# Optimization experiments

Measured on AMD Instinct MI355X. Metric: run time of the kernel, lower is better.

## Reference

```python
import jax, jax.numpy as jnp
import numpy as np

T, D, K, V, NB = 32768, 256, 16, 16, 2
H = K * V  # hidden size; must equal D for the residual x + y

def phi(x):
    return 1.0 + jax.nn.elu(x)

def _layernorm(x, w, b, eps=1e-5):
    m = x.mean(-1, keepdims=True)
    v = ((x - m) ** 2).mean(-1, keepdims=True)
    return (x - m) * jax.lax.rsqrt(v + eps) * w + b

def _combine(a, b):
    # reset-wrapped associative update: right element's start flag zeroes the left carry
    pa, sa, za = a
    pb, sb, zb = b
    keep = jnp.logical_not(pb)
    return (jnp.logical_or(pa, pb), keep * sa + sb, keep * za + zb)

def _block(x, start, s0, z0, Wk, Wq, Wv, bv, Wskip, bskip, Wm1, bm1, Wm2, bm2, Wm3, bm3, lnw, lnb):
    k = phi(x @ Wk.T)                                   # [T,K]
    q = phi(x @ Wq.T)                                   # [T,K]
    v = x @ Wv.T + bv                                   # [T,V]
    kv = jnp.einsum('ti,tj->tij', k, v)                 # [T,K,V]
    s = jnp.concatenate([s0, kv], axis=0)               # [T+1,K,V]
    z = jnp.concatenate([z0, k[:, None, :]], axis=0)    # [T+1,1,K]
    st = jnp.concatenate([jnp.zeros((1, 1, 1), bool), start.reshape(-1, 1, 1)], axis=0)
    _, s, z = jax.lax.associative_scan(_combine, (st, s, z), axis=0)
    s, z = s[1:], z[1:]
    numer = jnp.einsum('tij,ti->tj', s, q)              # [T,V]
    denom = jnp.einsum('tzi,tj->tz', z, q).clip(1e-6)   # [T,1] (faithful to source einsum)
    out = numer / denom                                 # [T,V]
    h = jax.nn.leaky_relu(out @ Wm1.T + bm1)
    h = jax.nn.leaky_relu(h @ Wm2.T + bm2)
    h = h @ Wm3.T + bm3
    return _layernorm(h + (x @ Wskip.T + bskip), lnw, lnb)

def _forward(x, start, s0, z0, Wk, Wq, Wv, bv, Wskip, bskip, Wm1, bm1, Wm2, bm2, Wm3, bm3, lnw, lnb):
    y = x
    for i in range(NB):  # small fixed layer loop
        y = _block(x, start, s0[i], z0[i], Wk[i], Wq[i], Wv[i], bv[i], Wskip[i], bskip[i],
                   Wm1[i], bm1[i], Wm2[i], bm2[i], Wm3[i], bm3[i], lnw[i], lnb[i])
        x = x + y
    return y

def setup_inputs() -> dict:
    key = jax.random.key(0)
    ks = jax.random.split(key, 12)
    g = lambda k, shp, fan: jax.random.normal(k, shp, jnp.float32) * (fan ** -0.5)
    return dict(
        x=jax.random.normal(ks[0], (T, D), jnp.float32),
        start=jax.random.randint(ks[1], (T,), 0, 2).astype(bool),
        s0=jnp.zeros((NB, 1, K, V), jnp.float32),
        z0=jnp.zeros((NB, 1, 1, K), jnp.float32),
        Wk=g(ks[2], (NB, K, D), D), Wq=g(ks[3], (NB, K, D), D),
        Wv=g(ks[4], (NB, V, D), D), bv=jnp.zeros((NB, V), jnp.float32),
        Wskip=g(ks[5], (NB, H, D), D), bskip=jnp.zeros((NB, H), jnp.float32),
        Wm1=g(ks[6], (NB, H, V), V), bm1=jnp.zeros((NB, H), jnp.float32),
        Wm2=g(ks[7], (NB, H, H), H), bm2=jnp.zeros((NB, H), jnp.float32),
        Wm3=g(ks[8], (NB, H, H), H), bm3=jnp.zeros((NB, H), jnp.float32),
        ln_w=jnp.ones((NB, H), jnp.float32), ln_b=jnp.zeros((NB, H), jnp.float32),
    )

def reference(x, start, s0, z0, Wk, Wq, Wv, bv, Wskip, bskip, Wm1, bm1, Wm2, bm2, Wm3, bm3, ln_w, ln_b):
    return _forward(x, start, s0, z0, Wk, Wq, Wv, bv, Wskip, bskip, Wm1, bm1, Wm2, bm2, Wm3, bm3, ln_w, ln_b)
```

## Files before the change

kernel.cpp:

```cpp
#include <hip/hip_runtime.h>
#include <hip/hip_bf16.h>
#include <cstdint>

#define TT   32768
#define DD   256
#define KV   16
#define NBLK 2
#define HH   256
#define CH   64
#define NCH  (TT / CH)

typedef __attribute__((ext_vector_type(8))) short bf16x8;
typedef __attribute__((ext_vector_type(4))) float f32x4;

__device__ __forceinline__ float phi_f(float x)  { return x > 0.f ? x + 1.f : expf(x); }
__device__ __forceinline__ float lrelu_f(float x){ return x > 0.f ? x : 0.01f * x; }
__device__ __forceinline__ unsigned short f2bf(float f) {
  unsigned u = __float_as_uint(f);
  u += 0x7fffu + ((u >> 16) & 1u);
  return (unsigned short)(u >> 16);
}
__device__ __forceinline__ float bf2f(unsigned short h) {
  return __uint_as_float(((unsigned)h) << 16);
}

__global__ void k_detect(const void* __restrict__ startp, int* __restrict__ flags) {
  int stride = gridDim.x * blockDim.x;
  for (int t = blockIdx.x * blockDim.x + threadIdx.x; t < TT / 4; t += stride) {
    unsigned u = ((const unsigned*)startp)[t];
    if (u > 1u) atomicOr(&flags[0], 1);
    float f = ((const float*)startp)[t];
    if (!(f == 0.f || f == 1.f)) atomicOr(&flags[1], 1);
  }
}

__global__ void k_canon(const void* __restrict__ startp, const int* __restrict__ flags,
                        float* __restrict__ start_f) {
  int v32 = flags[0], vf = flags[1];
  int stride = gridDim.x * blockDim.x;
  for (int t = blockIdx.x * blockDim.x + threadIdx.x; t < TT; t += stride) {
    bool s;
    if (v32 == 0)     s = ((const unsigned*)startp)[t] != 0u;
    else if (vf == 0) s = ((const float*)startp)[t] != 0.f;
    else              s = ((const unsigned char*)startp)[t] != 0;
    start_f[t] = s ? 1.f : 0.f;
  }
}

__global__ __launch_bounds__(256) void k_cvtbig(
    const float* __restrict__ s0, const float* __restrict__ s1, const float* __restrict__ s2,
    unsigned short* __restrict__ d0, unsigned short* __restrict__ d1,
    unsigned short* __restrict__ d2, int n) {
  int i = (blockIdx.x * 256 + threadIdx.x) * 8;
  const float* s; unsigned short* d;
  if (i < n)            { s = s0; d = d0; }
  else if (i < 2 * n)   { s = s1; d = d1; i -= n; }
  else if (i < 3 * n)   { s = s2; d = d2; i -= 2 * n; }
  else return;
  float4 a = *(const float4*)(s + i);
  float4 b = *(const float4*)(s + i + 4);
  float vals[8] = {a.x, a.y, a.z, a.w, b.x, b.y, b.z, b.w};
  bf16x8 t;
#pragma unroll
  for (int j = 0; j < 8; j++) t[j] = (short)f2bf(vals[j]);
  *(bf16x8*)(d + i) = t;
}

__global__ __launch_bounds__(256) void k_cvtproj(
    const float* __restrict__ Wk, const float* __restrict__ Wq, const float* __restrict__ Wv,
    unsigned short* __restrict__ wh, unsigned short* __restrict__ wl) {
  int t8 = blockIdx.x * 256 + threadIdx.x;
  if (t8 >= NBLK * 48 * 256 / 8) return;
  int e = t8 * 8;
  int b = e / (48 * 256);
  int rem = e - b * 48 * 256;
  int o = rem / (16 * 256);
  int nr = rem - o * 16 * 256;
  const float* src = (o == 0 ? Wk : o == 1 ? Wq : Wv) + b * 16 * 256 + nr;
  float4 a = *(const float4*)src;
  float4 c = *(const float4*)(src + 4);
  float vals[8] = {a.x, a.y, a.z, a.w, c.x, c.y, c.z, c.w};
  bf16x8 th, tl;
#pragma unroll
  for (int j = 0; j < 8; j++) {
    unsigned short h = f2bf(vals[j]);
    th[j] = (short)h;
    tl[j] = (short)f2bf(vals[j] - bf2f(h));
  }
  *(bf16x8*)(wh + e) = th;
  *(bf16x8*)(wl + e) = tl;
}

__global__ __launch_bounds__(256) void k_proj2(
    const float* __restrict__ x,
    const unsigned short* __restrict__ wh, const unsigned short* __restrict__ wl,
    const float* __restrict__ bv,
    float* __restrict__ kout, float* __restrict__ qout, float* __restrict__ vout) {
  __shared__ unsigned short xh[64 * 256];
  __shared__ unsigned short xl[64 * 256];
  int tid = threadIdx.x, wg = blockIdx.x;
  size_t rbase = (size_t)wg * 64;
  const float* xs = x + rbase * DD;
#pragma unroll
  for (int i = 0; i < 8; i++) {
    int idx = tid + i * 256;
    int row = idx >> 5, c8 = idx & 31;
    const float* p = xs + row * DD + c8 * 8;
    float4 a = *(const float4*)p;
    float4 b = *(const float4*)(p + 4);
    float vals[8] = {a.x, a.y, a.z, a.w, b.x, b.y, b.z, b.w};
    bf16x8 th, tl;
#pragma unroll
    for (int j = 0; j < 8; j++) {
      unsigned short h = f2bf(vals[j]);
      th[j] = (short)h;
      tl[j] = (short)f2bf(vals[j] - bf2f(h));
    }
    int off = row * 512 + ((c8 * 16) ^ ((row & 7) << 4));
    *(bf16x8*)((char*)xh + off) = th;
    *(bf16x8*)((char*)xl + off) = tl;
  }
  __syncthreads();

  int lane = tid & 63, wv = tid >> 6, lg = lane >> 4, lr = lane & 15;
  int r = wv * 16 + lr;
  f32x4 acc[3];
#pragma unroll
  for (int o = 0; o < 3; o++) acc[o] = (f32x4){0.f, 0.f, 0.f, 0.f};

#pragma unroll
  for (int kk = 0; kk < 8; kk++) {
    int kbyte = kk * 64 + lg * 16;
    int off = r * 512 + (kbyte ^ ((r & 7) << 4));
    bf16x8 ah = *(bf16x8*)((char*)xh + off);
    bf16x8 al = *(bf16x8*)((char*)xl + off);
#pragma unroll
    for (int o = 0; o < 3; o++) {
      bf16x8 bh = *(const bf16x8*)((const char*)wh + (o * 16 + lr) * 512 + kbyte);
      bf16x8 bl = *(const bf16x8*)((const char*)wl + (o * 16 + lr) * 512 + kbyte);
      acc[o] = __builtin_amdgcn_mfma_f32_16x16x32_bf16(ah, bh, acc[o], 0, 0, 0);
      acc[o] = __builtin_amdgcn_mfma_f32_16x16x32_bf16(al, bh, acc[o], 0, 0, 0);
      acc[o] = __builtin_amdgcn_mfma_f32_16x16x32_bf16(ah, bl, acc[o], 0, 0, 0);
    }
  }
  float bvv = bv[lr];
#pragma unroll
  for (int rg = 0; rg < 4; rg++) {
    size_t g = rbase + wv * 16 + lg * 4 + rg;
    kout[g * KV + lr] = phi_f(acc[0][rg]);
    qout[g * KV + lr] = phi_f(acc[1][rg]);
    vout[g * KV + lr] = acc[2][rg] + bvv;
  }
}

__global__ __launch_bounds__(256) void k_tails(
    const float* __restrict__ k, const float* __restrict__ v,
    const float* __restrict__ start_f,
    float* __restrict__ tails_s, float* __restrict__ tails_zs,
    float* __restrict__ tails_flag) {
  __shared__ float kc[CH * KV], vc[CH * KV], stc[CH], red[CH];
  __shared__ int lsS;
  int c = blockIdx.x, tid = threadIdx.x;
  const float* kp = k + (size_t)c * CH * KV;
  const float* vp = v + (size_t)c * CH * KV;
  for (int u = tid; u < CH * KV; u += 256) { kc[u] = kp[u]; vc[u] = vp[u]; }
  if (tid < CH) stc[tid] = start_f[c * CH + tid];
  __syncthreads();
  if (tid == 0) {
    int ls = -1;
    for (int t = 0; t < CH; t++) if (stc[t] != 0.f) ls = t;
    lsS = ls;
  }
  __syncthreads();
  int ls = lsS;
  int t0 = ls < 0 ? 0 : ls;
  int i = tid >> 4, j = tid & 15;
  float s = 0.f;
  for (int t = t0; t < CH; t++) s += kc[t * KV + i] * vc[t * KV + j];
  tails_s[(size_t)c * 256 + tid] = s;
  if (tid < CH) {
    float r = 0.f;
    if (tid >= t0) {
      for (int i2 = 0; i2 < KV; i2++) r += kc[tid * KV + i2];
    }
    red[tid] = r;
  }
  __syncthreads();
  if (tid == 0) {
    float z = 0.f;
    for (int t = 0; t < CH; t++) z += red[t];
    tails_zs[c] = z;
    tails_flag[c] = (ls >= 0) ? 1.f : 0.f;
  }
}

__global__ __launch_bounds__(256) void k_att(
    const float* __restrict__ q, const float* __restrict__ k,
    const float* __restrict__ v, const float* __restrict__ start_f,
    const float* __restrict__ tails_s, const float* __restrict__ tails_zs,
    const float* __restrict__ tails_flag,
    const float* __restrict__ s0, const float* __restrict__ z0,
    float* __restrict__ att) {
  __shared__ float qc[CH * KV], kc[CH * KV], vc[CH * KV], stc[CH];
  __shared__ float S[CH * CH];
  __shared__ float carry[256];
  __shared__ float ksum[CH], zsl[CH], qsum[CH];
  __shared__ int ns[CH];
  __shared__ float czs_s;
  int c = blockIdx.x, tid = threadIdx.x;
  size_t base = (size_t)c * CH * KV;
  for (int u = tid; u < CH * KV; u += 256) {
    qc[u] = q[base + u]; kc[u] = k[base + u]; vc[u] = v[base + u];
  }
  if (tid < CH) stc[tid] = start_f[c * CH + tid];
  __syncthreads();
  if (tid < CH) {
    int cnt = 0;
    for (int u = 0; u <= tid; u++) cnt += (stc[u] != 0.f);
    ns[tid] = cnt;
    float ks = 0.f, qs = 0.f;
    for (int i = 0; i < KV; i++) { ks += kc[tid * KV + i]; qs += qc[tid * KV + i]; }
    ksum[tid] = ks; qsum[tid] = qs;
  }
  __syncthreads();
  if (tid < CH) {
    float acc = 0.f;
    for (int u = tid; u >= 0; u--) { acc += ksum[u]; if (stc[u] != 0.f) break; }
    zsl[tid] = acc;
  }
  {
    float accs = 0.f, aczs = 0.f;
    int cc = c - 1;
    for (;;) {
      if (cc < 0) {
        accs += s0[tid];
        if (tid == 0) { float z = 0.f; for (int i = 0; i < KV; i++) z += z0[i]; aczs += z; }
        break;
      }
      float fl = tails_flag[cc];
      accs += tails_s[(size_t)cc * 256 + tid];
      if (tid == 0) aczs += tails_zs[cc];
      if (fl != 0.f) break;
      cc--;
    }
    carry[tid] = accs;
    if (tid == 0) czs_s = aczs;
  }
  __syncthreads();
  {
    int t = tid >> 2, g = tid & 3;
    for (int u = 0; u < 16; u++) {
      int tp = g * 16 + u;
      float val = 0.f;
      if (tp <= t && ns[tp] == ns[t]) {
        float dot = 0.f;
        for (int i = 0; i < KV; i++) dot += qc[t * KV + i] * kc[tp * KV + i];
        val = dot;
      }
      S[t * CH + tp] = val;
    }
  }
  __syncthreads();
  float czs = czs_s;
  int j = tid & 15, tr = tid >> 4;
  for (int p = 0; p < 4; p++) {
    int t = p * 16 + tr;
    float numer = 0.f;
    for (int tp = 0; tp < CH; tp++) numer += S[t * CH + tp] * vc[tp * KV + j];
    float zs = zsl[t];
    if (ns[t] == 0) {
      float cn = 0.f;
      for (int i = 0; i < KV; i++) cn += qc[t * KV + i] * carry[i * KV + j];
      numer += cn;
      zs += czs;
    }
    float denom = fmaxf(zs * qsum[t], 1e-6f);
    att[base + t * KV + j] = numer / denom;
  }
}

template<int WY, int WX>
__global__ __launch_bounds__(256, 2) void k_mlp2(
    const float* __restrict__ att, const float* __restrict__ xsrc,
    const float* __restrict__ Wm1, const float* __restrict__ bm1,
    const unsigned short* __restrict__ Wm2b, const float* __restrict__ bm2,
    const unsigned short* __restrict__ Wm3b, const float* __restrict__ bm3,
    const unsigned short* __restrict__ Wskb, const float* __restrict__ bsk,
    const float* __restrict__ lnw, const float* __restrict__ lnb,
    float* __restrict__ yout, float* __restrict__ xnext) {
  __shared__ unsigned short h1b[64 * 256];
  __shared__ unsigned short h2b[64 * 256];
  __shared__ float ao[64 * KV];
  __shared__ float lnwS[256], lnbS[256];
  __shared__ float redS[256], redQ[256];
  __shared__ float mrow[64], irow[64];

  int tid = threadIdx.x;
  int wg = blockIdx.x;
  size_t rbase = (size_t)wg * 64;

  for (int u = tid; u < 64 * KV; u += 256) ao[u] = att[rbase * KV + u];
  lnwS[tid] = lnw[tid];
  lnbS[tid] = lnb[tid];
  __syncthreads();

  {
    int jp = tid & 127;
    int rh = tid >> 7;
    float w0[16], w1[16];
#pragma unroll
    for (int c = 0; c < 16; c++) {
      w0[c] = Wm1[(2 * jp) * 16 + c];
      w1[c] = Wm1[(2 * jp + 1) * 16 + c];
    }
    float b0 = bm1[2 * jp], b1 = bm1[2 * jp + 1];
    for (int rr = 0; rr < 32; rr++) {
      int r = rh * 32 + rr;
      float a0 = b0, a1 = b1;
#pragma unroll
      for (int c = 0; c < 16; c++) {
        float xv = ao[r * 16 + c];
        a0 += xv * w0[c]; a1 += xv * w1[c];
      }
      a0 = lrelu_f(a0); a1 = lrelu_f(a1);
      unsigned pk = (unsigned)f2bf(a0) | ((unsigned)f2bf(a1) << 16);
      *(unsigned*)((char*)h1b + r * 512 + ((jp * 4) ^ ((r & 7) << 4))) = pk;
    }
  }
  __syncthreads();

  int lane = tid & 63;
  int wv = tid >> 6;
  int lg = lane >> 4;
  int lr = lane & 15;
  int nc0 = wv * 64;

  f32x4 acc[4][4];
#pragma unroll
  for (int a = 0; a < 4; a++)
#pragma unroll
    for (int b = 0; b < 4; b++) acc[a][b] = (f32x4){0.f, 0.f, 0.f, 0.f};

  for (int kk = 0; kk < 8; kk++) {
    int kbyte = kk * 64 + lg * 16;
    bf16x8 af[4], bfr[4];
#pragma unroll
    for (int mt = 0; mt < 4; mt++) {
      int r = mt * 16 + lr;
      af[mt] = *(bf16x8*)((char*)h1b + r * 512 + (kbyte ^ ((r & 7) << 4)));
    }
#pragma unroll
    for (int nt = 0; nt < 4; nt++) {
      int n = nc0 + nt * 16 + lr;
      bfr[nt] = *(const bf16x8*)((const char*)Wm2b + n * 512 + kbyte);
    }
#pragma unroll
    for (int mt = 0; mt < 4; mt++)
#pragma unroll
      for (int nt = 0; nt < 4; nt++)
        acc[mt][nt] = __builtin_amdgcn_mfma_f32_16x16x32_bf16(af[mt], bfr[nt], acc[mt][nt], 0, 0, 0);
  }
  {
    float bm2v[4];
#pragma unroll
    for (int nt = 0; nt < 4; nt++) bm2v[nt] = bm2[nc0 + nt * 16 + lr];
#pragma unroll
    for (int mt = 0; mt < 4; mt++)
#pragma unroll
      for (int nt = 0; nt < 4; nt++)
#pragma unroll
        for (int rg = 0; rg < 4; rg++) {
          int r = mt * 16 + lg * 4 + rg;
          int cc = nc0 + nt * 16 + lr;
          unsigned short hv = f2bf(lrelu_f(acc[mt][nt][rg] + bm2v[nt]));
          *(unsigned short*)((char*)h2b + r * 512 + ((cc * 2) ^ ((r & 7) << 4))) = hv;
        }
  }
  __syncthreads();

  f32x4 acc2[4][4];
#pragma unroll
  for (int a = 0; a < 4; a++)
#pragma unroll
    for (int b = 0; b < 4; b++) acc2[a][b] = (f32x4){0.f, 0.f, 0.f, 0.f};

  const float* xrow = xsrc + rbase * DD;
  for (int kk = 0; kk < 8; kk++) {
    int kbyte = kk * 64 + lg * 16;
    int kf = kk * 32 + lg * 8;
    bf16x8 a2[4], b3[4], bs[4], axv[4];
#pragma unroll
    for (int mt = 0; mt < 4; mt++) {
      int r = mt * 16 + lr;
      a2[mt] = *(bf16x8*)((char*)h2b + r * 512 + (kbyte ^ ((r & 7) << 4)));
    }
#pragma unroll
    for (int nt = 0; nt < 4; nt++) {
      int n = nc0 + nt * 16 + lr;
      b3[nt] = *(const bf16x8*)((const char*)Wm3b + n * 512 + kbyte);
      bs[nt] = *(const bf16x8*)((const char*)Wskb + n * 512 + kbyte);
    }
#pragma unroll
    for (int mt = 0; mt < 4; mt++) {
      const float* xp = xrow + (mt * 16 + lr) * DD + kf;
      float4 x0 = *(const float4*)xp;
      float4 x1 = *(const float4*)(xp + 4);
      bf16x8 t;
      t[0] = (short)f2bf(x0.x); t[1] = (short)f2bf(x0.y);
      t[2] = (short)f2bf(x0.z); t[3] = (short)f2bf(x0.w);
      t[4] = (short)f2bf(x1.x); t[5] = (short)f2bf(x1.y);
      t[6] = (short)f2bf(x1.z); t[7] = (short)f2bf(x1.w);
      axv[mt] = t;
    }
#pragma unroll
    for (int mt = 0; mt < 4; mt++)
#pragma unroll
      for (int nt = 0; nt < 4; nt++)
        acc2[mt][nt] = __builtin_amdgcn_mfma_f32_16x16x32_bf16(a2[mt], b3[nt], acc2[mt][nt], 0, 0, 0);
#pragma unroll
    for (int mt = 0; mt < 4; mt++)
#pragma unroll
      for (int nt = 0; nt < 4; nt++)
        acc2[mt][nt] = __builtin_amdgcn_mfma_f32_16x16x32_bf16(axv[mt], bs[nt], acc2[mt][nt], 0, 0, 0);
  }
#pragma unroll
  for (int nt = 0; nt < 4; nt++) {
    int cc = nc0 + nt * 16 + lr;
    float bb = bm3[cc] + bsk[cc];
#pragma unroll
    for (int mt = 0; mt < 4; mt++)
#pragma unroll
      for (int rg = 0; rg < 4; rg++) acc2[mt][nt][rg] += bb;
  }

#pragma unroll
  for (int mt = 0; mt < 4; mt++)
#pragma unroll
    for (int rg = 0; rg < 4; rg++) {
      float s = 0.f, q = 0.f;
#pragma unroll
      for (int nt = 0; nt < 4; nt++) {
        float v = acc2[mt][nt][rg];
        s += v; q += v * v;
      }
#pragma unroll
      for (int m = 1; m < 16; m <<= 1) {
        s += __shfl_xor(s, m);
        q += __shfl_xor(q, m);
      }
      if (lr == 0) {
        int r = mt * 16 + lg * 4 + rg;
        redS[wv * 64 + r] = s;
        redQ[wv * 64 + r] = q;
      }
    }
  __syncthreads();
  if (tid < 64) {
    float s = redS[tid] + redS[64 + tid] + redS[128 + tid] + redS[192 + tid];
    float q = redQ[tid] + redQ[64 + tid] + redQ[128 + tid] + redQ[192 + tid];
    float m = s * (1.f / 256.f);
    float var = q * (1.f / 256.f) - m * m;
    mrow[tid] = m;
    irow[tid] = rsqrtf(var + 1e-5f);
  }
  __syncthreads();

#pragma unroll
  for (int mt = 0; mt < 4; mt++)
#pragma unroll
    for (int rg = 0; rg < 4; rg++) {
      int r = mt * 16 + lg * 4 + rg;
      float m = mrow[r], is = irow[r];
      size_t gr = (rbase + r) * DD;
#pragma unroll
      for (int nt = 0; nt < 4; nt++) {
        int cc = nc0 + nt * 16 + lr;
        float val = acc2[mt][nt][rg];
        float y = (val - m) * is * lnwS[cc] + lnbS[cc];
        if (WY) yout[gr + cc] = y;
        if (WX) xnext[gr + cc] = xsrc[gr + cc] + y;
      }
    }
}

extern "C" void kernel_launch(void* const* d_in, const int* in_sizes, int n_in,
                              void* d_out, int out_size, void* d_ws, size_t ws_size,
                              hipStream_t stream) {
  const float* x_in = (const float*)d_in[0];
  const void*  startp = d_in[1];
  const float* s0  = (const float*)d_in[2];
  const float* z0  = (const float*)d_in[3];
  const float* Wk  = (const float*)d_in[4];
  const float* Wq  = (const float*)d_in[5];
  const float* Wv  = (const float*)d_in[6];
  const float* bv  = (const float*)d_in[7];
  const float* Wsk = (const float*)d_in[8];
  const float* bsk = (const float*)d_in[9];
  const float* Wm1 = (const float*)d_in[10];
  const float* bm1 = (const float*)d_in[11];
  const float* Wm2 = (const float*)d_in[12];
  const float* bm2 = (const float*)d_in[13];
  const float* Wm3 = (const float*)d_in[14];
  const float* bm3 = (const float*)d_in[15];
  const float* lnw = (const float*)d_in[16];
  const float* lnb = (const float*)d_in[17];
  float* yout = (float*)d_out;

  float* ws = (float*)d_ws;
  int*   flags   = (int*)d_ws;
  float* start_f = ws + 16;
  float* kbuf    = start_f + TT;
  float* qbuf    = kbuf + (size_t)TT * KV;
  float* vbuf    = qbuf + (size_t)TT * KV;
  float* abuf    = vbuf + (size_t)TT * KV;
  float* ts      = abuf + (size_t)TT * KV;
  float* tz      = ts + (size_t)NCH * 256;
  float* tf      = tz + NCH;
  float* xcur    = tf + NCH;
  unsigned short* wm2b  = (unsigned short*)(xcur + (size_t)TT * DD);
  unsigned short* wm3b  = wm2b + (size_t)NBLK * HH * HH;
  unsigned short* wskb  = wm3b + (size_t)NBLK * HH * HH;
  unsigned short* wpjh  = wskb + (size_t)NBLK * HH * DD;
  unsigned short* wpjl  = wpjh + (size_t)NBLK * 48 * DD;

  hipMemsetAsync(d_ws, 0, 64, stream);
  k_detect<<<64, 256, 0, stream>>>(startp, flags);
  k_canon<<<256, 256, 0, stream>>>(startp, flags, start_f);

  k_cvtbig<<<192, 256, 0, stream>>>(Wm2, Wm3, Wsk, wm2b, wm3b, wskb, NBLK * HH * HH);
  k_cvtproj<<<12, 256, 0, stream>>>(Wk, Wq, Wv, wpjh, wpjl);

  const float* xs = x_in;
  for (int b = 0; b < NBLK; b++) {
    k_proj2<<<TT / 64, 256, 0, stream>>>(xs,
        wpjh + (size_t)b * 48 * DD, wpjl + (size_t)b * 48 * DD,
        bv + (size_t)b * KV, kbuf, qbuf, vbuf);
    k_tails<<<NCH, 256, 0, stream>>>(kbuf, vbuf, start_f, ts, tz, tf);
    k_att<<<NCH, 256, 0, stream>>>(qbuf, kbuf, vbuf, start_f, ts, tz, tf,
        s0 + (size_t)b * 256, z0 + (size_t)b * KV, abuf);
    if (b == 0) {
      k_mlp2<0, 1><<<TT / 64, 256, 0, stream>>>(abuf, xs,
          Wm1 + (size_t)b * HH * KV, bm1 + (size_t)b * HH,
          wm2b + (size_t)b * HH * HH, bm2 + (size_t)b * HH,
          wm3b + (size_t)b * HH * HH, bm3 + (size_t)b * HH,
          wskb + (size_t)b * HH * DD, bsk + (size_t)b * HH,
          lnw + (size_t)b * HH, lnb + (size_t)b * HH,
          yout, xcur);
    } else {
      k_mlp2<1, 0><<<TT / 64, 256, 0, stream>>>(abuf, xs,
          Wm1 + (size_t)b * HH * KV, bm1 + (size_t)b * HH,
          wm2b + (size_t)b * HH * HH, bm2 + (size_t)b * HH,
          wm3b + (size_t)b * HH * HH, bm3 + (size_t)b * HH,
          wskb + (size_t)b * HH * DD, bsk + (size_t)b * HH,
          lnw + (size_t)b * HH, lnb + (size_t)b * HH,
          yout, xcur);
    }
    xs = xcur;
  }
}
```

Measured before the change: 291.6 us.

## Store activations as split bf16 hi/lo, MFMA first MLP layer, shrink LDS

The residual stream x is now kept in global memory as bf16 hi/lo pairs, written by a new up-front conversion kernel and updated in place by the MLP kernel. This removes the per-block fp32-to-bf16 conversion in the projection and MLP kernels. The first MLP layer moves from scalar FMA to split-bf16 MFMA with a zero-padded Wm1. LDS use in the MLP kernel shrinks through a single reused hidden buffer and a union, allowing 4 blocks per CU, and the attention score matrix is padded to avoid bank conflicts. The skip path now multiplies with the lo part of x as well, and x accumulates in split-bf16 form, which could change rounding slightly.

```diff
diff --git a/kernel.cpp b/kernel.cpp
--- a/kernel.cpp
+++ b/kernel.cpp
@@ -91,38 +91,56 @@
   *(bf16x8*)(wl + e) = tl;
 }
 
-__global__ __launch_bounds__(256) void k_proj2(
-    const float* __restrict__ x,
+__global__ __launch_bounds__(256) void k_cvtm1(
+    const float* __restrict__ Wm1,
+    unsigned short* __restrict__ h, unsigned short* __restrict__ l) {
+  int row = blockIdx.x * 256 + threadIdx.x;
+  if (row >= NBLK * 256) return;
+  const float* s = Wm1 + row * 16;
+  bf16x8 th0, tl0, th1, tl1, z;
+#pragma unroll
+  for (int j = 0; j < 8; j++) {
+    float v0 = s[j], v1 = s[j + 8];
+    unsigned short h0 = f2bf(v0), h1 = f2bf(v1);
+    th0[j] = (short)h0; tl0[j] = (short)f2bf(v0 - bf2f(h0));
+    th1[j] = (short)h1; tl1[j] = (short)f2bf(v1 - bf2f(h1));
+    z[j] = 0;
+  }
+  unsigned short* dh = h + row * 32;
+  unsigned short* dl = l + row * 32;
+  *(bf16x8*)(dh) = th0;  *(bf16x8*)(dh + 8) = th1;
+  *(bf16x8*)(dh + 16) = z; *(bf16x8*)(dh + 24) = z;
+  *(bf16x8*)(dl) = tl0;  *(bf16x8*)(dl + 8) = tl1;
+  *(bf16x8*)(dl + 16) = z; *(bf16x8*)(dl + 24) = z;
+}
+
+__global__ __launch_bounds__(256) void k_cvtx(const float* __restrict__ x,
+                                              unsigned short* __restrict__ xh,
+                                              unsigned short* __restrict__ xl) {
+  size_t i = ((size_t)blockIdx.x * 256 + threadIdx.x) * 8;
+  if (i >= (size_t)TT * DD) return;
+  float4 a = *(const float4*)(x + i);
+  float4 b = *(const float4*)(x + i + 4);
+  float vals[8] = {a.x, a.y, a.z, a.w, b.x, b.y, b.z, b.w};
+  bf16x8 th, tl;
+#pragma unroll
+  for (int j = 0; j < 8; j++) {
+    unsigned short h = f2bf(vals[j]);
+    th[j] = (short)h;
+    tl[j] = (short)f2bf(vals[j] - bf2f(h));
+  }
+  *(bf16x8*)(xh + i) = th;
+  *(bf16x8*)(xl + i) = tl;
+}
+
+__global__ __launch_bounds__(256) void k_proj3(
+    const unsigned short* __restrict__ xbh, const unsigned short* __restrict__ xbl,
     const unsigned short* __restrict__ wh, const unsigned short* __restrict__ wl,
     const float* __restrict__ bv,
     float* __restrict__ kout, float* __restrict__ qout, float* __restrict__ vout) {
-  __shared__ unsigned short xh[64 * 256];
-  __shared__ unsigned short xl[64 * 256];
   int tid = threadIdx.x, wg = blockIdx.x;
+  int lane = tid & 63, wv = tid >> 6, lg = lane >> 4, lr = lane & 15;
   size_t rbase = (size_t)wg * 64;
-  const float* xs = x + rbase * DD;
-#pragma unroll
-  for (int i = 0; i < 8; i++) {
-    int idx = tid + i * 256;
-    int row = idx >> 5, c8 = idx & 31;
-    const float* p = xs + row * DD + c8 * 8;
-    float4 a = *(const float4*)p;
-    float4 b = *(const float4*)(p + 4);
-    float vals[8] = {a.x, a.y, a.z, a.w, b.x, b.y, b.z, b.w};
-    bf16x8 th, tl;
-#pragma unroll
-    for (int j = 0; j < 8; j++) {
-      unsigned short h = f2bf(vals[j]);
-      th[j] = (short)h;
-      tl[j] = (short)f2bf(vals[j] - bf2f(h));
-    }
-    int off = row * 512 + ((c8 * 16) ^ ((row & 7) << 4));
-    *(bf16x8*)((char*)xh + off) = th;
-    *(bf16x8*)((char*)xl + off) = tl;
-  }
-  __syncthreads();
-
-  int lane = tid & 63, wv = tid >> 6, lg = lane >> 4, lr = lane & 15;
   int r = wv * 16 + lr;
   f32x4 acc[3];
 #pragma unroll
@@ -130,10 +148,10 @@
 
 #pragma unroll
   for (int kk = 0; kk < 8; kk++) {
+    size_t xo = (rbase + r) * DD + kk * 32 + lg * 8;
+    bf16x8 ah = *(const bf16x8*)(xbh + xo);
+    bf16x8 al = *(const bf16x8*)(xbl + xo);
     int kbyte = kk * 64 + lg * 16;
-    int off = r * 512 + (kbyte ^ ((r & 7) << 4));
-    bf16x8 ah = *(bf16x8*)((char*)xh + off);
-    bf16x8 al = *(bf16x8*)((char*)xl + off);
 #pragma unroll
     for (int o = 0; o < 3; o++) {
       bf16x8 bh = *(const bf16x8*)((const char*)wh + (o * 16 + lr) * 512 + kbyte);
@@ -194,6 +212,7 @@
   }
 }
 
+#define SP 65
 __global__ __launch_bounds__(256) void k_att(
     const float* __restrict__ q, const float* __restrict__ k,
     const float* __restrict__ v, const float* __restrict__ start_f,
@@ -202,7 +221,7 @@
     const float* __restrict__ s0, const float* __restrict__ z0,
     float* __restrict__ att) {
   __shared__ float qc[CH * KV], kc[CH * KV], vc[CH * KV], stc[CH];
-  __shared__ float S[CH * CH];
+  __shared__ float S[CH * SP];
   __shared__ float carry[256];
   __shared__ float ksum[CH], zsl[CH], qsum[CH];
   __shared__ int ns[CH];
@@ -257,7 +276,7 @@
         for (int i = 0; i < KV; i++) dot += qc[t * KV + i] * kc[tp * KV + i];
         val = dot;
       }
-      S[t * CH + tp] = val;
+      S[t * SP + tp] = val;
     }
   }
   __syncthreads();
@@ -266,7 +285,7 @@
   for (int p = 0; p < 4; p++) {
     int t = p * 16 + tr;
     float numer = 0.f;
-    for (int tp = 0; tp < CH; tp++) numer += S[t * CH + tp] * vc[tp * KV + j];
+    for (int tp = 0; tp < CH; tp++) numer += S[t * SP + tp] * vc[tp * KV + j];
     float zs = zsl[t];
     if (ns[t] == 0) {
       float cn = 0.f;
@@ -280,86 +299,108 @@
 }
 
 template<int WY, int WX>
-__global__ __launch_bounds__(256, 2) void k_mlp2(
-    const float* __restrict__ att, const float* __restrict__ xsrc,
-    const float* __restrict__ Wm1, const float* __restrict__ bm1,
+__global__ __launch_bounds__(256, 4) void k_mlp3(
+    const float* __restrict__ att,
+    unsigned short* __restrict__ xbh, unsigned short* __restrict__ xbl,
+    const unsigned short* __restrict__ wm1h, const unsigned short* __restrict__ wm1l,
+    const float* __restrict__ bm1,
     const unsigned short* __restrict__ Wm2b, const float* __restrict__ bm2,
     const unsigned short* __restrict__ Wm3b, const float* __restrict__ bm3,
     const unsigned short* __restrict__ Wskb, const float* __restrict__ bsk,
     const float* __restrict__ lnw, const float* __restrict__ lnb,
-    float* __restrict__ yout, float* __restrict__ xnext) {
-  __shared__ unsigned short h1b[64 * 256];
-  __shared__ unsigned short h2b[64 * 256];
-  __shared__ float ao[64 * KV];
-  __shared__ float lnwS[256], lnbS[256];
-  __shared__ float redS[256], redQ[256];
-  __shared__ float mrow[64], irow[64];
-
-  int tid = threadIdx.x;
-  int wg = blockIdx.x;
+    float* __restrict__ yout) {
+  __shared__ unsigned short hb[64 * 256];
+  __shared__ __align__(16) char uni[8192];
+  unsigned short* aoh = (unsigned short*)uni;
+  unsigned short* aol = aoh + 64 * 32;
+  float* redS = (float*)uni;
+  float* redQ = redS + 256;
+  float* mrow = redQ + 256;
+  float* irow = mrow + 64;
+
+  int tid = threadIdx.x, wg = blockIdx.x;
   size_t rbase = (size_t)wg * 64;
 
-  for (int u = tid; u < 64 * KV; u += 256) ao[u] = att[rbase * KV + u];
-  lnwS[tid] = lnw[tid];
-  lnbS[tid] = lnb[tid];
-  __syncthreads();
+  for (int idx = tid; idx < 64 * 32; idx += 256) {
+    int row = idx >> 5, col = idx & 31;
+    float v = (col < 16) ? att[(rbase + row) * KV + col] : 0.f;
+    unsigned short h = f2bf(v);
+    aoh[idx] = h;
+    aol[idx] = f2bf(v - bf2f(h));
+  }
+  __syncthreads();
+
+  int lane = tid & 63, wv = tid >> 6, lg = lane >> 4, lr = lane & 15;
+  int nc0 = wv * 64;
+
+  f32x4 acc[4][4];
+#pragma unroll
+  for (int a = 0; a < 4; a++)
+#pragma unroll
+    for (int b = 0; b < 4; b++) acc[a][b] = (f32x4){0.f, 0.f, 0.f, 0.f};
 
   {
-    int jp = tid & 127;
-    int rh = tid >> 7;
-    float w0[16], w1[16];
-#pragma unroll
-    for (int c = 0; c < 16; c++) {
-      w0[c] = Wm1[(2 * jp) * 16 + c];
-      w1[c] = Wm1[(2 * jp + 1) * 16 + c];
-    }
-    float b0 = bm1[2 * jp], b1 = bm1[2 * jp + 1];
-    for (int rr = 0; rr < 32; rr++) {
-      int r = rh * 32 + rr;
-      float a0 = b0, a1 = b1;
-#pragma unroll
-      for (int c = 0; c < 16; c++) {
-        float xv = ao[r * 16 + c];
-        a0 += xv * w0[c]; a1 += xv * w1[c];
+    bf16x8 b1h[4], b1l[4];
+#pragma unroll
+    for (int nt = 0; nt < 4; nt++) {
+      int n = nc0 + nt * 16 + lr;
+      b1h[nt] = *(const bf16x8*)(wm1h + n * 32 + lg * 8);
+      b1l[nt] = *(const bf16x8*)(wm1l + n * 32 + lg * 8);
+    }
+#pragma unroll
+    for (int mt = 0; mt < 4; mt++) {
+      int r = mt * 16 + lr;
+      bf16x8 ah = *(bf16x8*)(aoh + r * 32 + lg * 8);
+      bf16x8 al = *(bf16x8*)(aol + r * 32 + lg * 8);
+#pragma unroll
+      for (int nt = 0; nt < 4; nt++) {
+        acc[mt][nt] = __builtin_amdgcn_mfma_f32_16x16x32_bf16(ah, b1h[nt], acc[mt][nt], 0, 0, 0);
+        acc[mt][nt] = __builtin_amdgcn_mfma_f32_16x16x32_bf16(al, b1h[nt], acc[mt][nt], 0, 0, 0);
+        acc[mt][nt] = __builtin_amdgcn_mfma_f32_16x16x32_bf16(ah, b1l[nt], acc[mt][nt], 0, 0, 0);
       }
-      a0 = lrelu_f(a0); a1 = lrelu_f(a1);
-      unsigned pk = (unsigned)f2bf(a0) | ((unsigned)f2bf(a1) << 16);
-      *(unsigned*)((char*)h1b + r * 512 + ((jp * 4) ^ ((r & 7) << 4))) = pk;
-    }
-  }
-  __syncthreads();
-
-  int lane = tid & 63;
-  int wv = tid >> 6;
-  int lg = lane >> 4;
-  int lr = lane & 15;
-  int nc0 = wv * 64;
-
-  f32x4 acc[4][4];
+    }
+  }
+  __syncthreads();
+  {
+    float bm1v[4];
+#pragma unroll
+    for (int nt = 0; nt < 4; nt++) bm1v[nt] = bm1[nc0 + nt * 16 + lr];
+#pragma unroll
+    for (int mt = 0; mt < 4; mt++)
+#pragma unroll
+      for (int nt = 0; nt < 4; nt++)
+#pragma unroll
+        for (int rg = 0; rg < 4; rg++) {
+          int r = mt * 16 + lg * 4 + rg;
+          int cc = nc0 + nt * 16 + lr;
+          *(unsigned short*)((char*)hb + r * 512 + ((cc * 2) ^ ((r & 7) << 4))) =
+              f2bf(lrelu_f(acc[mt][nt][rg] + bm1v[nt]));
+        }
+  }
+  __syncthreads();
+
 #pragma unroll
   for (int a = 0; a < 4; a++)
 #pragma unroll
     for (int b = 0; b < 4; b++) acc[a][b] = (f32x4){0.f, 0.f, 0.f, 0.f};
-
   for (int kk = 0; kk < 8; kk++) {
     int kbyte = kk * 64 + lg * 16;
-    bf16x8 af[4], bfr[4];
-#pragma unroll
-    for (int mt = 0; mt < 4; mt++) {
-      int r = mt * 16 + lr;
-      af[mt] = *(bf16x8*)((char*)h1b + r * 512 + (kbyte ^ ((r & 7) << 4)));
-    }
+    bf16x8 bfr[4];
 #pragma unroll
     for (int nt = 0; nt < 4; nt++) {
       int n = nc0 + nt * 16 + lr;
       bfr[nt] = *(const bf16x8*)((const char*)Wm2b + n * 512 + kbyte);
     }
 #pragma unroll
-    for (int mt = 0; mt < 4; mt++)
+    for (int mt = 0; mt < 4; mt++) {
+      int r = mt * 16 + lr;
+      bf16x8 af = *(bf16x8*)((char*)hb + r * 512 + (kbyte ^ ((r & 7) << 4)));
 #pragma unroll
       for (int nt = 0; nt < 4; nt++)
-        acc[mt][nt] = __builtin_amdgcn_mfma_f32_16x16x32_bf16(af[mt], bfr[nt], acc[mt][nt], 0, 0, 0);
-  }
+        acc[mt][nt] = __builtin_amdgcn_mfma_f32_16x16x32_bf16(af, bfr[nt], acc[mt][nt], 0, 0, 0);
+    }
+  }
+  __syncthreads();
   {
     float bm2v[4];
 #pragma unroll
@@ -372,8 +413,8 @@
         for (int rg = 0; rg < 4; rg++) {
           int r = mt * 16 + lg * 4 + rg;
           int cc = nc0 + nt * 16 + lr;
-          unsigned short hv = f2bf(lrelu_f(acc[mt][nt][rg] + bm2v[nt]));
-          *(unsigned short*)((char*)h2b + r * 512 + ((cc * 2) ^ ((r & 7) << 4))) = hv;
+          *(unsigned short*)((char*)hb + r * 512 + ((cc * 2) ^ ((r & 7) << 4))) =
+              f2bf(lrelu_f(acc[mt][nt][rg] + bm2v[nt]));
         }
   }
   __syncthreads();
@@ -383,17 +424,9 @@
   for (int a = 0; a < 4; a++)
 #pragma unroll
     for (int b = 0; b < 4; b++) acc2[a][b] = (f32x4){0.f, 0.f, 0.f, 0.f};
-
-  const float* xrow = xsrc + rbase * DD;
   for (int kk = 0; kk < 8; kk++) {
     int kbyte = kk * 64 + lg * 16;
-    int kf = kk * 32 + lg * 8;
-    bf16x8 a2[4], b3[4], bs[4], axv[4];
-#pragma unroll
-    for (int mt = 0; mt < 4; mt++) {
-      int r = mt * 16 + lr;
-      a2[mt] = *(bf16x8*)((char*)h2b + r * 512 + (kbyte ^ ((r & 7) << 4)));
-    }
+    bf16x8 b3[4], bs[4];
 #pragma unroll
     for (int nt = 0; nt < 4; nt++) {
       int n = nc0 + nt * 16 + lr;
@@ -402,26 +435,21 @@
     }
 #pragma unroll
     for (int mt = 0; mt < 4; mt++) {
-      const float* xp = xrow + (mt * 16 + lr) * DD + kf;
-      float4 x0 = *(const float4*)xp;
-      float4 x1 = *(const float4*)(xp + 4);
-      bf16x8 t;
-      t[0] = (short)f2bf(x0.x); t[1] = (short)f2bf(x0.y);
-      t[2] = (short)f2bf(x0.z); t[3] = (short)f2bf(x0.w);
-      t[4] = (short)f2bf(x1.x); t[5] = (short)f2bf(x1.y);
-      t[6] = (short)f2bf(x1.z); t[7] = (short)f2bf(x1.w);
-      axv[mt] = t;
-    }
-#pragma unroll
-    for (int mt = 0; mt < 4; mt++)
+      int r = mt * 16 + lr;
+      bf16x8 a2 = *(bf16x8*)((char*)hb + r * 512 + (kbyte ^ ((r & 7) << 4)));
 #pragma unroll
       for (int nt = 0; nt < 4; nt++)
-        acc2[mt][nt] = __builtin_amdgcn_mfma_f32_16x16x32_bf16(a2[mt], b3[nt], acc2[mt][nt], 0, 0, 0);
-#pragma unroll
-    for (int mt = 0; mt < 4; mt++)
+        acc2[mt][nt] = __builtin_amdgcn_mfma_f32_16x16x32_bf16(a2, b3[nt], acc2[mt][nt], 0, 0, 0);
+      size_t xo = (rbase + r) * DD + kk * 32 + lg * 8;
+      bf16x8 xh8 = *(const bf16x8*)(xbh + xo);
 #pragma unroll
       for (int nt = 0; nt < 4; nt++)
-        acc2[mt][nt] = __builtin_amdgcn_mfma_f32_16x16x32_bf16(axv[mt], bs[nt], acc2[mt][nt], 0, 0, 0);
+        acc2[mt][nt] = __builtin_amdgcn_mfma_f32_16x16x32_bf16(xh8, bs[nt], acc2[mt][nt], 0, 0, 0);
+      bf16x8 xl8 = *(const bf16x8*)(xbl + xo);
+#pragma unroll
+      for (int nt = 0; nt < 4; nt++)
+        acc2[mt][nt] = __builtin_amdgcn_mfma_f32_16x16x32_bf16(xl8, bs[nt], acc2[mt][nt], 0, 0, 0);
+    }
   }
 #pragma unroll
   for (int nt = 0; nt < 4; nt++) {
@@ -465,22 +493,36 @@
   }
   __syncthreads();
 
-#pragma unroll
-  for (int mt = 0; mt < 4; mt++)
-#pragma unroll
-    for (int rg = 0; rg < 4; rg++) {
-      int r = mt * 16 + lg * 4 + rg;
-      float m = mrow[r], is = irow[r];
-      size_t gr = (rbase + r) * DD;
-#pragma unroll
-      for (int nt = 0; nt < 4; nt++) {
-        int cc = nc0 + nt * 16 + lr;
-        float val = acc2[mt][nt][rg];
-        float y = (val - m) * is * lnwS[cc] + lnbS[cc];
-        if (WY) yout[gr + cc] = y;
-        if (WX) xnext[gr + cc] = xsrc[gr + cc] + y;
+  {
+    float lnwv[4], lnbv[4];
+#pragma unroll
+    for (int nt = 0; nt < 4; nt++) {
+      int cc = nc0 + nt * 16 + lr;
+      lnwv[nt] = lnw[cc]; lnbv[nt] = lnb[cc];
+    }
+#pragma unroll
+    for (int mt = 0; mt < 4; mt++)
+#pragma unroll
+      for (int rg = 0; rg < 4; rg++) {
+        int r = mt * 16 + lg * 4 + rg;
+        float m = mrow[r], is = irow[r];
+        size_t gr = (rbase + r) * DD;
+#pragma unroll
+        for (int nt = 0; nt < 4; nt++) {
+          int cc = nc0 + nt * 16 + lr;
+          float y = (acc2[mt][nt][rg] - m) * is * lnwv[nt] + lnbv[nt];
+          if (WY) yout[gr + cc] = y;
+          if (WX) {
+            size_t o = gr + cc;
+            float xf = bf2f(xbh[o]) + bf2f(xbl[o]);
+            float s = xf + y;
+            unsigned short nh = f2bf(s);
+            xbh[o] = nh;
+            xbl[o] = f2bf(s - bf2f(nh));
+          }
+        }
       }
-    }
+  }
 }
 
 extern "C" void kernel_launch(void* const* d_in, const int* in_sizes, int n_in,
@@ -516,12 +558,15 @@
   float* ts      = abuf + (size_t)TT * KV;
   float* tz      = ts + (size_t)NCH * 256;
   float* tf      = tz + NCH;
-  float* xcur    = tf + NCH;
-  unsigned short* wm2b  = (unsigned short*)(xcur + (size_t)TT * DD);
-  unsigned short* wm3b  = wm2b + (size_t)NBLK * HH * HH;
-  unsigned short* wskb  = wm3b + (size_t)NBLK * HH * HH;
-  unsigned short* wpjh  = wskb + (size_t)NBLK * HH * DD;
-  unsigned short* wpjl  = wpjh + (size_t)NBLK * 48 * DD;
+  unsigned short* wm2b = (unsigned short*)(tf + NCH);
+  unsigned short* wm3b = wm2b + (size_t)NBLK * HH * HH;
+  unsigned short* wskb = wm3b + (size_t)NBLK * HH * HH;
+  unsigned short* wpjh = wskb + (size_t)NBLK * HH * DD;
+  unsigned short* wpjl = wpjh + (size_t)NBLK * 48 * DD;
+  unsigned short* wm1h = wpjl + (size_t)NBLK * 48 * DD;
+  unsigned short* wm1l = wm1h + (size_t)NBLK * HH * 32;
+  unsigned short* xbh  = wm1l + (size_t)NBLK * HH * 32;
+  unsigned short* xbl  = xbh + (size_t)TT * DD;
 
   hipMemsetAsync(d_ws, 0, 64, stream);
   k_detect<<<64, 256, 0, stream>>>(startp, flags);
@@ -529,32 +574,30 @@
 
   k_cvtbig<<<192, 256, 0, stream>>>(Wm2, Wm3, Wsk, wm2b, wm3b, wskb, NBLK * HH * HH);
   k_cvtproj<<<12, 256, 0, stream>>>(Wk, Wq, Wv, wpjh, wpjl);
-
-  const float* xs = x_in;
+  k_cvtm1<<<2, 256, 0, stream>>>(Wm1, wm1h, wm1l);
+  k_cvtx<<<TT * DD / 8 / 256, 256, 0, stream>>>(x_in, xbh, xbl);
+
   for (int b = 0; b < NBLK; b++) {
-    k_proj2<<<TT / 64, 256, 0, stream>>>(xs,
+    k_proj3<<<TT / 64, 256, 0, stream>>>(xbh, xbl,
         wpjh + (size_t)b * 48 * DD, wpjl + (size_t)b * 48 * DD,
         bv + (size_t)b * KV, kbuf, qbuf, vbuf);
     k_tails<<<NCH, 256, 0, stream>>>(kbuf, vbuf, start_f, ts, tz, tf);
     k_att<<<NCH, 256, 0, stream>>>(qbuf, kbuf, vbuf, start_f, ts, tz, tf,
         s0 + (size_t)b * 256, z0 + (size_t)b * KV, abuf);
     if (b == 0) {
-      k_mlp2<0, 1><<<TT / 64, 256, 0, stream>>>(abuf, xs,
-          Wm1 + (size_t)b * HH * KV, bm1 + (size_t)b * HH,
+      k_mlp3<0, 1><<<TT / 64, 256, 0, stream>>>(abuf, xbh, xbl,
+          wm1h + (size_t)b * HH * 32, wm1l + (size_t)b * HH * 32, bm1 + (size_t)b * HH,
           wm2b + (size_t)b * HH * HH, bm2 + (size_t)b * HH,
           wm3b + (size_t)b * HH * HH, bm3 + (size_t)b * HH,
           wskb + (size_t)b * HH * DD, bsk + (size_t)b * HH,
-          lnw + (size_t)b * HH, lnb + (size_t)b * HH,
-          yout, xcur);
+          lnw + (size_t)b * HH, lnb + (size_t)b * HH, yout);
     } else {
-      k_mlp2<1, 0><<<TT / 64, 256, 0, stream>>>(abuf, xs,
-          Wm1 + (size_t)b * HH * KV, bm1 + (size_t)b * HH,
+      k_mlp3<1, 0><<<TT / 64, 256, 0, stream>>>(abuf, xbh, xbl,
+          wm1h + (size_t)b * HH * 32, wm1l + (size_t)b * HH * 32, bm1 + (size_t)b * HH,
           wm2b + (size_t)b * HH * HH, bm2 + (size_t)b * HH,
           wm3b + (size_t)b * HH * HH, bm3 + (size_t)b * HH,
           wskb + (size_t)b * HH * DD, bsk + (size_t)b * HH,
-          lnw + (size_t)b * HH, lnb + (size_t)b * HH,
-          yout, xcur);
-    }
-    xs = xcur;
-  }
-}
+          lnw + (size_t)b * HH, lnb + (size_t)b * HH, yout);
+    }
+  }
+}
```

New measurement: 394.0 us. 35.1% more time.
